# Optimization experiments

Measured on AMD Instinct MI355X. Metric: run time of the kernel, lower is better.

The kernel has to match this reference:

```python
import jax, jax.numpy as jnp
import numpy as np

NUM_CLASSES = 100            # num_classes (no-object class index == NUM_CLASSES)
MIN_PAIR_W = 0.1             # min_point_pair_weight
EPS = 1e-8


def setup_inputs() -> dict:
    key = jax.random.key(0)
    ks = jax.random.split(key, 8)
    B, Q, C1 = 16, 200, NUM_CLASSES + 1
    M = 800                  # matched GT instances across the batch
    NPTS = 200000            # sampled pixel points (per-point query-logit vectors)
    P = 500000               # point pairs for the clustering loss
    pred_logits = jax.random.normal(ks[0], (B, Q, C1), dtype=jnp.float32)
    targets = jax.random.randint(ks[1], (M,), 0, NUM_CLASSES)
    idx_b = jax.random.randint(ks[2], (M,), 0, B)
    idx_q = jax.random.randint(ks[3], (M,), 0, Q)
    src_clusters = jax.random.normal(ks[4], (NPTS, Q), dtype=jnp.float32)
    pairs = jax.random.randint(ks[5], (P, 2), 0, NPTS)
    pair_pos = jax.random.bernoulli(ks[6], 0.5, (P,))
    pair_weights = jax.random.uniform(ks[7], (P,), dtype=jnp.float32)
    # empty_weight buffer: ones with eos_coef on the no-object class
    empty_weight = jnp.ones((C1,), dtype=jnp.float32).at[-1].set(0.1)
    return {"pred_logits": pred_logits, "targets": targets, "idx_b": idx_b,
            "idx_q": idx_q, "src_clusters": src_clusters, "pairs": pairs,
            "pair_pos": pair_pos, "pair_weights": pair_weights,
            "empty_weight": empty_weight}


def _loss_labels(pred_logits, targets, idx_b, idx_q, empty_weight):
    B, Q, _ = pred_logits.shape
    # target_classes = full(no-object); target_classes[indices] = targets
    target_classes = jnp.full((B, Q), NUM_CLASSES, dtype=jnp.int32)
    target_classes = target_classes.at[idx_b, idx_q].set(targets.astype(jnp.int32))
    logp = jax.nn.log_softmax(pred_logits.astype(jnp.float32), axis=-1)  # [B,Q,C+1]
    nll = -jnp.take_along_axis(logp, target_classes[..., None], axis=-1)[..., 0]
    w = empty_weight[target_classes]
    # torch weighted cross_entropy: sum(w*nll)/sum(w)
    return jnp.sum(w * nll) / jnp.sum(w)


def _loss_clusters(src_clusters, pairs, pair_pos, pair_weights):
    a = src_clusters[pairs[:, 0]]            # [P,Q] gather
    b = src_clusters[pairs[:, 1]]            # [P,Q] gather
    cos = jnp.sum(a * b, axis=-1) / (
        jnp.linalg.norm(a, axis=-1) * jnp.linalg.norm(b, axis=-1) + EPS)
    w = jnp.maximum(pair_weights, MIN_PAIR_W)
    per_pair = jnp.where(pair_pos, 1.0 - cos, jnp.maximum(cos, 0.0))
    return jnp.sum(w * per_pair) / jnp.sum(w)


def reference(pred_logits, targets, idx_b, idx_q, src_clusters, pairs,
              pair_pos, pair_weights, empty_weight):
    loss_ce = _loss_labels(pred_logits, targets, idx_b, idx_q, empty_weight)
    loss_cluster = _loss_clusters(src_clusters, pairs, pair_pos, pair_weights)
    return loss_ce + loss_cluster
```

## Files before the change

kernel.cpp:

```cpp
#include <hip/hip_runtime.h>
#include <math.h>

#define NUM_CLASSES_ 100
#define C1_ 101
#define BQ_ 3200
#define QDIM_ 200
#define ROW_DW 64

typedef __attribute__((ext_vector_type(4))) int i32x4;

__global__ void init_kernel(float* acc, int* tc) {
    int i = blockIdx.x * blockDim.x + threadIdx.x;
    if (i < 4) acc[i] = 0.0f;
    if (i < BQ_) tc[i] = -1;
}

__global__ void scatter_kernel(const int* __restrict__ targets,
                               const int* __restrict__ idx_b,
                               const int* __restrict__ idx_q,
                               int* tc, int M) {
    int m = blockIdx.x * blockDim.x + threadIdx.x;
    if (m < M) {
        int slot = idx_b[m] * QDIM_ + idx_q[m];
        atomicMax(&tc[slot], (m << 8) | targets[m]);
    }
}

__global__ __launch_bounds__(256) void ce_kernel(const float* __restrict__ logits,
                                                 const int* __restrict__ tc,
                                                 const float* __restrict__ empty_w,
                                                 float* acc) {
    int lane = threadIdx.x & 63;
    int gw = (blockIdx.x * blockDim.x + threadIdx.x) >> 6;
    int nw = (gridDim.x * blockDim.x) >> 6;
    float lnum = 0.0f, lden = 0.0f;
    for (int row = gw; row < BQ_; row += nw) {
        const float* x = logits + (size_t)row * C1_;
        float x0 = x[lane];
        bool has2 = (lane < C1_ - 64);
        float x1 = has2 ? x[lane + 64] : -INFINITY;
        float m = fmaxf(x0, x1);
        #pragma unroll
        for (int off = 32; off; off >>= 1) m = fmaxf(m, __shfl_xor(m, off));
        float s = expf(x0 - m) + (has2 ? expf(x1 - m) : 0.0f);
        #pragma unroll
        for (int off = 32; off; off >>= 1) s += __shfl_xor(s, off);
        int packed = tc[row];
        int cls = (packed >= 0) ? (packed & 255) : NUM_CLASSES_;
        float xt = x[cls];
        float nll = -(xt - m - logf(s));
        float w = empty_w[cls];
        lnum += w * nll;
        lden += w;
    }
    if (lane == 0) { atomicAdd(&acc[0], lnum); atomicAdd(&acc[1], lden); }
}

__global__ __launch_bounds__(256) void quantize_kernel(const float* __restrict__ src,
                                                       unsigned int* __restrict__ qtab,
                                                       float* __restrict__ invq, int npts) {
    int lane = threadIdx.x & 63;
    int gw = (blockIdx.x * blockDim.x + threadIdx.x) >> 6;
    int nw = (gridDim.x * blockDim.x) >> 6;
    for (int r = gw; r < npts; r += nw) {
        float4 a = make_float4(0.f, 0.f, 0.f, 0.f);
        float s = 0.0f;
        if (lane < QDIM_ / 4) {
            a = reinterpret_cast<const float4*>(src + (size_t)r * QDIM_)[lane];
            s = a.x * a.x + a.y * a.y + a.z * a.z + a.w * a.w;
        }
        #pragma unroll
        for (int off = 32; off; off >>= 1) s += __shfl_xor(s, off);
        float inv = rsqrtf(s);
        inv = inv * (1.5f - 0.5f * s * inv * inv);
        float sc = inv * 127.0f;
        int q0 = (int)rintf(a.x * sc);
        int q1 = (int)rintf(a.y * sc);
        int q2 = (int)rintf(a.z * sc);
        int q3 = (int)rintf(a.w * sc);
        unsigned int packed = (unsigned)(q0 & 255) | ((unsigned)(q1 & 255) << 8)
                            | ((unsigned)(q2 & 255) << 16) | ((unsigned)(q3 & 255) << 24);
        int sq = q0 * q0 + q1 * q1 + q2 * q2 + q3 * q3;
        #pragma unroll
        for (int off = 32; off; off >>= 1) sq += __shfl_xor(sq, off);
        qtab[(size_t)r * ROW_DW + lane] = (lane < QDIM_ / 4) ? packed : 0u;
        if (lane == 0) {
            float fs = (float)sq;
            float iv = rsqrtf(fs);
            iv = iv * (1.5f - 0.5f * fs * iv * iv);
            invq[r] = iv;
        }
    }
}

__global__ __launch_bounds__(256) void pair_mfma_kernel(const uint4* __restrict__ qtab4,
                                                        const int2* __restrict__ pairs2,
                                                        const int* __restrict__ pos,
                                                        const float* __restrict__ pw,
                                                        const float* __restrict__ invq,
                                                        float* acc, int P) {
    int lane = threadIdx.x & 63;
    int i15 = lane & 15;
    int grp = lane >> 4;
    int gw = (blockIdx.x * blockDim.x + threadIdx.x) >> 6;
    int nw = (gridDim.x * blockDim.x) >> 6;
    int nchunks = (P + 15) / 16;

    int myreg = i15 - (grp << 2);
    bool owns = (myreg >= 0) && (myreg < 4);

    float num = 0.0f, den = 0.0f;

    int pA; int2 prA; uint4 a0A, a1A, a2A, a3A, b0A, b1A, b2A, b3A;
    int posA; float pwA, iqA;
    int pB; int2 prB; uint4 a0B, a1B, a2B, a3B, b0B, b1B, b2B, b3B;
    int posB; float pwB, iqB;

    auto loadA = [&](int c) {
        pA = c * 16 + i15;
        int pc = min(pA, P - 1);
        prA = pairs2[pc];
        const uint4* ar = qtab4 + (size_t)prA.x * 16;
        const uint4* br = qtab4 + (size_t)prA.y * 16;
        a0A = ar[grp]; a1A = ar[4 + grp]; a2A = ar[8 + grp]; a3A = ar[12 + grp];
        b0A = br[grp]; b1A = br[4 + grp]; b2A = br[8 + grp]; b3A = br[12 + grp];
        posA = pos[pc]; pwA = pw[pc];
        iqA = invq[prA.x] * invq[prA.y];
    };
    auto loadB = [&](int c) {
        pB = c * 16 + i15;
        int pc = min(pB, P - 1);
        prB = pairs2[pc];
        const uint4* ar = qtab4 + (size_t)prB.x * 16;
        const uint4* br = qtab4 + (size_t)prB.y * 16;
        a0B = ar[grp]; a1B = ar[4 + grp]; a2B = ar[8 + grp]; a3B = ar[12 + grp];
        b0B = br[grp]; b1B = br[4 + grp]; b2B = br[8 + grp]; b3B = br[12 + grp];
        posB = pos[pc]; pwB = pw[pc];
        iqB = invq[prB.x] * invq[prB.y];
    };
    auto procA = [&]() {
        i32x4 macc = {0, 0, 0, 0};
        macc = __builtin_amdgcn_mfma_i32_16x16x64_i8(*(i32x4*)&a0A, *(i32x4*)&b0A, macc, 0, 0, 0);
        macc = __builtin_amdgcn_mfma_i32_16x16x64_i8(*(i32x4*)&a1A, *(i32x4*)&b1A, macc, 0, 0, 0);
        macc = __builtin_amdgcn_mfma_i32_16x16x64_i8(*(i32x4*)&a2A, *(i32x4*)&b2A, macc, 0, 0, 0);
        macc = __builtin_amdgcn_mfma_i32_16x16x64_i8(*(i32x4*)&a3A, *(i32x4*)&b3A, macc, 0, 0, 0);
        if (owns && pA < P) {
            int d = (myreg == 0) ? macc[0] : (myreg == 1) ? macc[1]
                  : (myreg == 2) ? macc[2] : macc[3];
            float cosv = (float)d * iqA;
            float per = posA ? (1.0f - cosv) : fmaxf(cosv, 0.0f);
            float w = fmaxf(pwA, 0.1f);
            num += w * per;
            den += w;
        }
    };
    auto procB = [&]() {
        i32x4 macc = {0, 0, 0, 0};
        macc = __builtin_amdgcn_mfma_i32_16x16x64_i8(*(i32x4*)&a0B, *(i32x4*)&b0B, macc, 0, 0, 0);
        macc = __builtin_amdgcn_mfma_i32_16x16x64_i8(*(i32x4*)&a1B, *(i32x4*)&b1B, macc, 0, 0, 0);
        macc = __builtin_amdgcn_mfma_i32_16x16x64_i8(*(i32x4*)&a2B, *(i32x4*)&b2B, macc, 0, 0, 0);
        macc = __builtin_amdgcn_mfma_i32_16x16x64_i8(*(i32x4*)&a3B, *(i32x4*)&b3B, macc, 0, 0, 0);
        if (owns && pB < P) {
            int d = (myreg == 0) ? macc[0] : (myreg == 1) ? macc[1]
                  : (myreg == 2) ? macc[2] : macc[3];
            float cosv = (float)d * iqB;
            float per = posB ? (1.0f - cosv) : fmaxf(cosv, 0.0f);
            float w = fmaxf(pwB, 0.1f);
            num += w * per;
            den += w;
        }
    };

    if (gw < nchunks) {
        loadA(gw);
        int c = gw;
        for (;;) {
            int cB = c + nw;
            bool hasB = (cB < nchunks);
            if (hasB) loadB(cB);
            procA();
            if (!hasB) break;
            int cA = cB + nw;
            bool hasA = (cA < nchunks);
            if (hasA) loadA(cA);
            procB();
            if (!hasA) break;
            c = cA;
        }
    }

    #pragma unroll
    for (int off = 32; off; off >>= 1) {
        num += __shfl_xor(num, off);
        den += __shfl_xor(den, off);
    }
    __shared__ float snum[4], sden[4];
    int wib = threadIdx.x >> 6;
    if (lane == 0) { snum[wib] = num; sden[wib] = den; }
    __syncthreads();
    if (threadIdx.x == 0) {
        atomicAdd(&acc[2], snum[0] + snum[1] + snum[2] + snum[3]);
        atomicAdd(&acc[3], sden[0] + sden[1] + sden[2] + sden[3]);
    }
}

__global__ __launch_bounds__(256) void pair_fp32_kernel(const float* __restrict__ src,
                                                        const int* __restrict__ pairs,
                                                        const int* __restrict__ pos,
                                                        const float* __restrict__ pw,
                                                        float* acc, int P) {
    int lane = threadIdx.x & 63;
    int gw = (blockIdx.x * blockDim.x + threadIdx.x) >> 6;
    int nw = (gridDim.x * blockDim.x) >> 6;
    float num = 0.0f, den = 0.0f;
    for (int p = gw; p < P; p += nw) {
        int2 pr = reinterpret_cast<const int2*>(pairs)[p];
        float dot = 0.0f, saa = 0.0f, sbb = 0.0f;
        if (lane < QDIM_ / 4) {
            float4 a = reinterpret_cast<const float4*>(src + (size_t)pr.x * QDIM_)[lane];
            float4 b = reinterpret_cast<const float4*>(src + (size_t)pr.y * QDIM_)[lane];
            dot = a.x * b.x + a.y * b.y + a.z * b.z + a.w * b.w;
            saa = a.x * a.x + a.y * a.y + a.z * a.z + a.w * a.w;
            sbb = b.x * b.x + b.y * b.y + b.z * b.z + b.w * b.w;
        }
        #pragma unroll
        for (int off = 32; off; off >>= 1) {
            dot += __shfl_xor(dot, off);
            saa += __shfl_xor(saa, off);
            sbb += __shfl_xor(sbb, off);
        }
        float cosv = dot / (sqrtf(saa) * sqrtf(sbb) + 1e-8f);
        float per = pos[p] ? (1.0f - cosv) : fmaxf(cosv, 0.0f);
        float w = fmaxf(pw[p], 0.1f);
        num += w * per;
        den += w;
    }
    __shared__ float snum[4], sden[4];
    int wib = threadIdx.x >> 6;
    if (lane == 0) { snum[wib] = num; sden[wib] = den; }
    __syncthreads();
    if (threadIdx.x == 0) {
        atomicAdd(&acc[2], snum[0] + snum[1] + snum[2] + snum[3]);
        atomicAdd(&acc[3], sden[0] + sden[1] + sden[2] + sden[3]);
    }
}

__global__ void final_kernel(const float* __restrict__ acc, float* out) {
    if (threadIdx.x == 0 && blockIdx.x == 0)
        out[0] = acc[0] / acc[1] + acc[2] / acc[3];
}

extern "C" void kernel_launch(void* const* d_in, const int* in_sizes, int n_in,
                              void* d_out, int out_size, void* d_ws, size_t ws_size,
                              hipStream_t stream) {
    const float* pred_logits = (const float*)d_in[0];
    const int*   targets     = (const int*)d_in[1];
    const int*   idx_b       = (const int*)d_in[2];
    const int*   idx_q       = (const int*)d_in[3];
    const float* src         = (const float*)d_in[4];
    const int*   pairs       = (const int*)d_in[5];
    const int*   pair_pos    = (const int*)d_in[6];
    const float* pair_w      = (const float*)d_in[7];
    const float* empty_w     = (const float*)d_in[8];
    float* out = (float*)d_out;

    int M = in_sizes[1];
    int P = in_sizes[7];
    int npts = in_sizes[4] / QDIM_;

    float* acc = (float*)d_ws;
    int*   tc  = (int*)((char*)d_ws + 16);
    unsigned int* qtab = (unsigned int*)((char*)d_ws + 16384);
    float* invq = (float*)((char*)d_ws + 16384 + (size_t)npts * 256);

    init_kernel<<<(BQ_ + 255) / 256, 256, 0, stream>>>(acc, tc);
    scatter_kernel<<<(M + 255) / 256, 256, 0, stream>>>(targets, idx_b, idx_q, tc, M);
    ce_kernel<<<200, 256, 0, stream>>>(pred_logits, tc, empty_w, acc);

    bool i8 = ws_size >= (size_t)16384 + (size_t)npts * 256 + (size_t)npts * 4;
    if (i8) {
        quantize_kernel<<<2048, 256, 0, stream>>>(src, qtab, invq, npts);
        pair_mfma_kernel<<<2048, 256, 0, stream>>>((const uint4*)qtab, (const int2*)pairs,
                                                   pair_pos, pair_w, invq, acc, P);
    } else {
        pair_fp32_kernel<<<2048, 256, 0, stream>>>(src, pairs, pair_pos, pair_w, acc, P);
    }
    final_kernel<<<1, 64, 0, stream>>>(acc, out);
}
```

Before: 349.7 us.

## Bucket pairs by first point and map buckets to XCDs for L2 locality

Adds a histogram, prefix-sum and scatter pass that reorders the point pairs by the high bits of their first index. The pair kernel then assigns contiguous ranges of sorted chunks to each XCD (blockIdx & 7), so gathers of the quantized rows hit in that XCD's L2. The CE kernel is fused into the quantize launch as extra blocks, and the target scatter is merged with the histogram. The cost is three extra passes over the pair arrays with atomics, plus extra workspace.

```diff
diff --git a/kernel.cpp b/kernel.cpp
--- a/kernel.cpp
+++ b/kernel.cpp
@@ -9,20 +9,243 @@
 
 typedef __attribute__((ext_vector_type(4))) int i32x4;
 
-__global__ void init_kernel(float* acc, int* tc) {
+__global__ void init_kernel(float* acc, int* tc, int* cnt, int nb) {
     int i = blockIdx.x * blockDim.x + threadIdx.x;
     if (i < 4) acc[i] = 0.0f;
     if (i < BQ_) tc[i] = -1;
-}
-
-__global__ void scatter_kernel(const int* __restrict__ targets,
-                               const int* __restrict__ idx_b,
-                               const int* __restrict__ idx_q,
-                               int* tc, int M) {
-    int m = blockIdx.x * blockDim.x + threadIdx.x;
-    if (m < M) {
-        int slot = idx_b[m] * QDIM_ + idx_q[m];
-        atomicMax(&tc[slot], (m << 8) | targets[m]);
+    if (i < nb) cnt[i] = 0;
+}
+
+__global__ void scatter_hist_kernel(const int* __restrict__ targets,
+                                    const int* __restrict__ idx_b,
+                                    const int* __restrict__ idx_q,
+                                    int* tc, int M,
+                                    const int2* __restrict__ pairs2,
+                                    int* cnt, int shift, int P) {
+    int t = blockIdx.x * blockDim.x + threadIdx.x;
+    if (t < M) {
+        int slot = idx_b[t] * QDIM_ + idx_q[t];
+        atomicMax(&tc[slot], (t << 8) | targets[t]);
+    }
+    int stride = gridDim.x * blockDim.x;
+    for (int p = t; p < P; p += stride)
+        atomicAdd(&cnt[pairs2[p].x >> shift], 1);
+}
+
+__global__ void prefix_kernel(const int* __restrict__ cnt, int* cursor, int nb) {
+    __shared__ int s[256];
+    int tid = threadIdx.x;
+    int v = (tid < nb) ? cnt[tid] : 0;
+    s[tid] = v;
+    __syncthreads();
+    #pragma unroll
+    for (int off = 1; off < 256; off <<= 1) {
+        int t = (tid >= off) ? s[tid - off] : 0;
+        __syncthreads();
+        s[tid] += t;
+        __syncthreads();
+    }
+    if (tid < nb) cursor[tid] = s[tid] - v;
+}
+
+__global__ void scatter_pairs_kernel(const int2* __restrict__ pairs2,
+                                     const int* __restrict__ pos,
+                                     const float* __restrict__ pw,
+                                     int* cursor, int shift,
+                                     int2* __restrict__ sp,
+                                     int* __restrict__ spos,
+                                     float* __restrict__ spw, int P) {
+    int t = blockIdx.x * blockDim.x + threadIdx.x;
+    int stride = gridDim.x * blockDim.x;
+    for (int p = t; p < P; p += stride) {
+        int2 pr = pairs2[p];
+        int slot = atomicAdd(&cursor[pr.x >> shift], 1);
+        sp[slot] = pr;
+        spos[slot] = pos[p];
+        spw[slot] = pw[p];
+    }
+}
+
+__global__ __launch_bounds__(256) void quant_ce_kernel(const float* __restrict__ src,
+                                                       unsigned int* __restrict__ qtab,
+                                                       float* __restrict__ invq, int npts,
+                                                       const float* __restrict__ logits,
+                                                       const int* __restrict__ tc,
+                                                       const float* __restrict__ empty_w,
+                                                       float* acc, int qblocks) {
+    int lane = threadIdx.x & 63;
+    if ((int)blockIdx.x < qblocks) {
+        int gw = (blockIdx.x * blockDim.x + threadIdx.x) >> 6;
+        int nw = (qblocks * blockDim.x) >> 6;
+        for (int r = gw; r < npts; r += nw) {
+            float4 a = make_float4(0.f, 0.f, 0.f, 0.f);
+            float s = 0.0f;
+            if (lane < QDIM_ / 4) {
+                a = reinterpret_cast<const float4*>(src + (size_t)r * QDIM_)[lane];
+                s = a.x * a.x + a.y * a.y + a.z * a.z + a.w * a.w;
+            }
+            #pragma unroll
+            for (int off = 32; off; off >>= 1) s += __shfl_xor(s, off);
+            float inv = rsqrtf(s);
+            inv = inv * (1.5f - 0.5f * s * inv * inv);
+            float sc = inv * 127.0f;
+            int q0 = (int)rintf(a.x * sc);
+            int q1 = (int)rintf(a.y * sc);
+            int q2 = (int)rintf(a.z * sc);
+            int q3 = (int)rintf(a.w * sc);
+            unsigned int packed = (unsigned)(q0 & 255) | ((unsigned)(q1 & 255) << 8)
+                                | ((unsigned)(q2 & 255) << 16) | ((unsigned)(q3 & 255) << 24);
+            int sq = q0 * q0 + q1 * q1 + q2 * q2 + q3 * q3;
+            #pragma unroll
+            for (int off = 32; off; off >>= 1) sq += __shfl_xor(sq, off);
+            qtab[(size_t)r * ROW_DW + lane] = (lane < QDIM_ / 4) ? packed : 0u;
+            if (lane == 0) {
+                float fs = (float)sq;
+                float iv = rsqrtf(fs);
+                iv = iv * (1.5f - 0.5f * fs * iv * iv);
+                invq[r] = iv;
+            }
+        }
+    } else {
+        int bid = blockIdx.x - qblocks;
+        int gw = (bid * blockDim.x + threadIdx.x) >> 6;
+        int nw = (200 * blockDim.x) >> 6;
+        float lnum = 0.0f, lden = 0.0f;
+        for (int row = gw; row < BQ_; row += nw) {
+            const float* x = logits + (size_t)row * C1_;
+            float x0 = x[lane];
+            bool has2 = (lane < C1_ - 64);
+            float x1 = has2 ? x[lane + 64] : -INFINITY;
+            float m = fmaxf(x0, x1);
+            #pragma unroll
+            for (int off = 32; off; off >>= 1) m = fmaxf(m, __shfl_xor(m, off));
+            float s = expf(x0 - m) + (has2 ? expf(x1 - m) : 0.0f);
+            #pragma unroll
+            for (int off = 32; off; off >>= 1) s += __shfl_xor(s, off);
+            int packed = tc[row];
+            int cls = (packed >= 0) ? (packed & 255) : NUM_CLASSES_;
+            float xt = x[cls];
+            float nll = -(xt - m - logf(s));
+            float w = empty_w[cls];
+            lnum += w * nll;
+            lden += w;
+        }
+        if (lane == 0) { atomicAdd(&acc[0], lnum); atomicAdd(&acc[1], lden); }
+    }
+}
+
+__global__ __launch_bounds__(256) void pair_mfma_kernel(const uint4* __restrict__ qtab4,
+                                                        const int2* __restrict__ pairs2,
+                                                        const int* __restrict__ pos,
+                                                        const float* __restrict__ pw,
+                                                        const float* __restrict__ invq,
+                                                        float* acc, int P) {
+    int lane = threadIdx.x & 63;
+    int i15 = lane & 15;
+    int grp = lane >> 4;
+    int wib = threadIdx.x >> 6;
+    int nchunks = (P + 15) / 16;
+
+    int xcd = blockIdx.x & 7;
+    int lb  = blockIdx.x >> 3;
+    int lw  = lb * 4 + wib;
+    int lnw = ((gridDim.x >> 3) * blockDim.x) >> 6;
+    int nxc = (nchunks + 7) / 8;
+    int cbeg = xcd * nxc;
+    int cend = min(nchunks, cbeg + nxc);
+
+    int myreg = i15 - (grp << 2);
+    bool owns = (myreg >= 0) && (myreg < 4);
+
+    float num = 0.0f, den = 0.0f;
+
+    int pA; uint4 a0A, a1A, a2A, a3A, b0A, b1A, b2A, b3A; int posA; float pwA, iqA;
+    int pB; uint4 a0B, a1B, a2B, a3B, b0B, b1B, b2B, b3B; int posB; float pwB, iqB;
+
+    auto loadA = [&](int c) {
+        pA = c * 16 + i15;
+        int pc = min(pA, P - 1);
+        int2 pr = pairs2[pc];
+        const uint4* ar = qtab4 + (size_t)pr.x * 16;
+        const uint4* br = qtab4 + (size_t)pr.y * 16;
+        a0A = ar[grp]; a1A = ar[4 + grp]; a2A = ar[8 + grp]; a3A = ar[12 + grp];
+        b0A = br[grp]; b1A = br[4 + grp]; b2A = br[8 + grp]; b3A = br[12 + grp];
+        posA = pos[pc]; pwA = pw[pc];
+        iqA = invq[pr.x] * invq[pr.y];
+    };
+    auto loadB = [&](int c) {
+        pB = c * 16 + i15;
+        int pc = min(pB, P - 1);
+        int2 pr = pairs2[pc];
+        const uint4* ar = qtab4 + (size_t)pr.x * 16;
+        const uint4* br = qtab4 + (size_t)pr.y * 16;
+        a0B = ar[grp]; a1B = ar[4 + grp]; a2B = ar[8 + grp]; a3B = ar[12 + grp];
+        b0B = br[grp]; b1B = br[4 + grp]; b2B = br[8 + grp]; b3B = br[12 + grp];
+        posB = pos[pc]; pwB = pw[pc];
+        iqB = invq[pr.x] * invq[pr.y];
+    };
+    auto procA = [&]() {
+        i32x4 macc = {0, 0, 0, 0};
+        macc = __builtin_amdgcn_mfma_i32_16x16x64_i8(*(i32x4*)&a0A, *(i32x4*)&b0A, macc, 0, 0, 0);
+        macc = __builtin_amdgcn_mfma_i32_16x16x64_i8(*(i32x4*)&a1A, *(i32x4*)&b1A, macc, 0, 0, 0);
+        macc = __builtin_amdgcn_mfma_i32_16x16x64_i8(*(i32x4*)&a2A, *(i32x4*)&b2A, macc, 0, 0, 0);
+        macc = __builtin_amdgcn_mfma_i32_16x16x64_i8(*(i32x4*)&a3A, *(i32x4*)&b3A, macc, 0, 0, 0);
+        if (owns && pA < P) {
+            int d = (myreg == 0) ? macc[0] : (myreg == 1) ? macc[1]
+                  : (myreg == 2) ? macc[2] : macc[3];
+            float cosv = (float)d * iqA;
+            float per = posA ? (1.0f - cosv) : fmaxf(cosv, 0.0f);
+            float w = fmaxf(pwA, 0.1f);
+            num += w * per;
+            den += w;
+        }
+    };
+    auto procB = [&]() {
+        i32x4 macc = {0, 0, 0, 0};
+        macc = __builtin_amdgcn_mfma_i32_16x16x64_i8(*(i32x4*)&a0B, *(i32x4*)&b0B, macc, 0, 0, 0);
+        macc = __builtin_amdgcn_mfma_i32_16x16x64_i8(*(i32x4*)&a1B, *(i32x4*)&b1B, macc, 0, 0, 0);
+        macc = __builtin_amdgcn_mfma_i32_16x16x64_i8(*(i32x4*)&a2B, *(i32x4*)&b2B, macc, 0, 0, 0);
+        macc = __builtin_amdgcn_mfma_i32_16x16x64_i8(*(i32x4*)&a3B, *(i32x4*)&b3B, macc, 0, 0, 0);
+        if (owns && pB < P) {
+            int d = (myreg == 0) ? macc[0] : (myreg == 1) ? macc[1]
+                  : (myreg == 2) ? macc[2] : macc[3];
+            float cosv = (float)d * iqB;
+            float per = posB ? (1.0f - cosv) : fmaxf(cosv, 0.0f);
+            float w = fmaxf(pwB, 0.1f);
+            num += w * per;
+            den += w;
+        }
+    };
+
+    int c = cbeg + lw;
+    if (c < cend) {
+        loadA(c);
+        for (;;) {
+            int cB = c + lnw;
+            bool hasB = (cB < cend);
+            if (hasB) loadB(cB);
+            procA();
+            if (!hasB) break;
+            int cA = cB + lnw;
+            bool hasA = (cA < cend);
+            if (hasA) loadA(cA);
+            procB();
+            if (!hasA) break;
+            c = cA;
+        }
+    }
+
+    #pragma unroll
+    for (int off = 32; off; off >>= 1) {
+        num += __shfl_xor(num, off);
+        den += __shfl_xor(den, off);
+    }
+    __shared__ float snum[4], sden[4];
+    if (lane == 0) { snum[wib] = num; sden[wib] = den; }
+    __syncthreads();
+    if (threadIdx.x == 0) {
+        atomicAdd(&acc[2], snum[0] + snum[1] + snum[2] + snum[3]);
+        atomicAdd(&acc[3], sden[0] + sden[1] + sden[2] + sden[3]);
     }
 }
 
@@ -56,154 +279,6 @@
     if (lane == 0) { atomicAdd(&acc[0], lnum); atomicAdd(&acc[1], lden); }
 }
 
-__global__ __launch_bounds__(256) void quantize_kernel(const float* __restrict__ src,
-                                                       unsigned int* __restrict__ qtab,
-                                                       float* __restrict__ invq, int npts) {
-    int lane = threadIdx.x & 63;
-    int gw = (blockIdx.x * blockDim.x + threadIdx.x) >> 6;
-    int nw = (gridDim.x * blockDim.x) >> 6;
-    for (int r = gw; r < npts; r += nw) {
-        float4 a = make_float4(0.f, 0.f, 0.f, 0.f);
-        float s = 0.0f;
-        if (lane < QDIM_ / 4) {
-            a = reinterpret_cast<const float4*>(src + (size_t)r * QDIM_)[lane];
-            s = a.x * a.x + a.y * a.y + a.z * a.z + a.w * a.w;
-        }
-        #pragma unroll
-        for (int off = 32; off; off >>= 1) s += __shfl_xor(s, off);
-        float inv = rsqrtf(s);
-        inv = inv * (1.5f - 0.5f * s * inv * inv);
-        float sc = inv * 127.0f;
-        int q0 = (int)rintf(a.x * sc);
-        int q1 = (int)rintf(a.y * sc);
-        int q2 = (int)rintf(a.z * sc);
-        int q3 = (int)rintf(a.w * sc);
-        unsigned int packed = (unsigned)(q0 & 255) | ((unsigned)(q1 & 255) << 8)
-                            | ((unsigned)(q2 & 255) << 16) | ((unsigned)(q3 & 255) << 24);
-        int sq = q0 * q0 + q1 * q1 + q2 * q2 + q3 * q3;
-        #pragma unroll
-        for (int off = 32; off; off >>= 1) sq += __shfl_xor(sq, off);
-        qtab[(size_t)r * ROW_DW + lane] = (lane < QDIM_ / 4) ? packed : 0u;
-        if (lane == 0) {
-            float fs = (float)sq;
-            float iv = rsqrtf(fs);
-            iv = iv * (1.5f - 0.5f * fs * iv * iv);
-            invq[r] = iv;
-        }
-    }
-}
-
-__global__ __launch_bounds__(256) void pair_mfma_kernel(const uint4* __restrict__ qtab4,
-                                                        const int2* __restrict__ pairs2,
-                                                        const int* __restrict__ pos,
-                                                        const float* __restrict__ pw,
-                                                        const float* __restrict__ invq,
-                                                        float* acc, int P) {
-    int lane = threadIdx.x & 63;
-    int i15 = lane & 15;
-    int grp = lane >> 4;
-    int gw = (blockIdx.x * blockDim.x + threadIdx.x) >> 6;
-    int nw = (gridDim.x * blockDim.x) >> 6;
-    int nchunks = (P + 15) / 16;
-
-    int myreg = i15 - (grp << 2);
-    bool owns = (myreg >= 0) && (myreg < 4);
-
-    float num = 0.0f, den = 0.0f;
-
-    int pA; int2 prA; uint4 a0A, a1A, a2A, a3A, b0A, b1A, b2A, b3A;
-    int posA; float pwA, iqA;
-    int pB; int2 prB; uint4 a0B, a1B, a2B, a3B, b0B, b1B, b2B, b3B;
-    int posB; float pwB, iqB;
-
-    auto loadA = [&](int c) {
-        pA = c * 16 + i15;
-        int pc = min(pA, P - 1);
-        prA = pairs2[pc];
-        const uint4* ar = qtab4 + (size_t)prA.x * 16;
-        const uint4* br = qtab4 + (size_t)prA.y * 16;
-        a0A = ar[grp]; a1A = ar[4 + grp]; a2A = ar[8 + grp]; a3A = ar[12 + grp];
-        b0A = br[grp]; b1A = br[4 + grp]; b2A = br[8 + grp]; b3A = br[12 + grp];
-        posA = pos[pc]; pwA = pw[pc];
-        iqA = invq[prA.x] * invq[prA.y];
-    };
-    auto loadB = [&](int c) {
-        pB = c * 16 + i15;
-        int pc = min(pB, P - 1);
-        prB = pairs2[pc];
-        const uint4* ar = qtab4 + (size_t)prB.x * 16;
-        const uint4* br = qtab4 + (size_t)prB.y * 16;
-        a0B = ar[grp]; a1B = ar[4 + grp]; a2B = ar[8 + grp]; a3B = ar[12 + grp];
-        b0B = br[grp]; b1B = br[4 + grp]; b2B = br[8 + grp]; b3B = br[12 + grp];
-        posB = pos[pc]; pwB = pw[pc];
-        iqB = invq[prB.x] * invq[prB.y];
-    };
-    auto procA = [&]() {
-        i32x4 macc = {0, 0, 0, 0};
-        macc = __builtin_amdgcn_mfma_i32_16x16x64_i8(*(i32x4*)&a0A, *(i32x4*)&b0A, macc, 0, 0, 0);
-        macc = __builtin_amdgcn_mfma_i32_16x16x64_i8(*(i32x4*)&a1A, *(i32x4*)&b1A, macc, 0, 0, 0);
-        macc = __builtin_amdgcn_mfma_i32_16x16x64_i8(*(i32x4*)&a2A, *(i32x4*)&b2A, macc, 0, 0, 0);
-        macc = __builtin_amdgcn_mfma_i32_16x16x64_i8(*(i32x4*)&a3A, *(i32x4*)&b3A, macc, 0, 0, 0);
-        if (owns && pA < P) {
-            int d = (myreg == 0) ? macc[0] : (myreg == 1) ? macc[1]
-                  : (myreg == 2) ? macc[2] : macc[3];
-            float cosv = (float)d * iqA;
-            float per = posA ? (1.0f - cosv) : fmaxf(cosv, 0.0f);
-            float w = fmaxf(pwA, 0.1f);
-            num += w * per;
-            den += w;
-        }
-    };
-    auto procB = [&]() {
-        i32x4 macc = {0, 0, 0, 0};
-        macc = __builtin_amdgcn_mfma_i32_16x16x64_i8(*(i32x4*)&a0B, *(i32x4*)&b0B, macc, 0, 0, 0);
-        macc = __builtin_amdgcn_mfma_i32_16x16x64_i8(*(i32x4*)&a1B, *(i32x4*)&b1B, macc, 0, 0, 0);
-        macc = __builtin_amdgcn_mfma_i32_16x16x64_i8(*(i32x4*)&a2B, *(i32x4*)&b2B, macc, 0, 0, 0);
-        macc = __builtin_amdgcn_mfma_i32_16x16x64_i8(*(i32x4*)&a3B, *(i32x4*)&b3B, macc, 0, 0, 0);
-        if (owns && pB < P) {
-            int d = (myreg == 0) ? macc[0] : (myreg == 1) ? macc[1]
-                  : (myreg == 2) ? macc[2] : macc[3];
-            float cosv = (float)d * iqB;
-            float per = posB ? (1.0f - cosv) : fmaxf(cosv, 0.0f);
-            float w = fmaxf(pwB, 0.1f);
-            num += w * per;
-            den += w;
-        }
-    };
-
-    if (gw < nchunks) {
-        loadA(gw);
-        int c = gw;
-        for (;;) {
-            int cB = c + nw;
-            bool hasB = (cB < nchunks);
-            if (hasB) loadB(cB);
-            procA();
-            if (!hasB) break;
-            int cA = cB + nw;
-            bool hasA = (cA < nchunks);
-            if (hasA) loadA(cA);
-            procB();
-            if (!hasA) break;
-            c = cA;
-        }
-    }
-
-    #pragma unroll
-    for (int off = 32; off; off >>= 1) {
-        num += __shfl_xor(num, off);
-        den += __shfl_xor(den, off);
-    }
-    __shared__ float snum[4], sden[4];
-    int wib = threadIdx.x >> 6;
-    if (lane == 0) { snum[wib] = num; sden[wib] = den; }
-    __syncthreads();
-    if (threadIdx.x == 0) {
-        atomicAdd(&acc[2], snum[0] + snum[1] + snum[2] + snum[3]);
-        atomicAdd(&acc[3], sden[0] + sden[1] + sden[2] + sden[3]);
-    }
-}
-
 __global__ __launch_bounds__(256) void pair_fp32_kernel(const float* __restrict__ src,
                                                         const int* __restrict__ pairs,
                                                         const int* __restrict__ pos,
@@ -268,21 +343,39 @@
     int P = in_sizes[7];
     int npts = in_sizes[4] / QDIM_;
 
-    float* acc = (float*)d_ws;
-    int*   tc  = (int*)((char*)d_ws + 16);
-    unsigned int* qtab = (unsigned int*)((char*)d_ws + 16384);
-    float* invq = (float*)((char*)d_ws + 16384 + (size_t)npts * 256);
-
-    init_kernel<<<(BQ_ + 255) / 256, 256, 0, stream>>>(acc, tc);
-    scatter_kernel<<<(M + 255) / 256, 256, 0, stream>>>(targets, idx_b, idx_q, tc, M);
-    ce_kernel<<<200, 256, 0, stream>>>(pred_logits, tc, empty_w, acc);
-
-    bool i8 = ws_size >= (size_t)16384 + (size_t)npts * 256 + (size_t)npts * 4;
-    if (i8) {
-        quantize_kernel<<<2048, 256, 0, stream>>>(src, qtab, invq, npts);
-        pair_mfma_kernel<<<2048, 256, 0, stream>>>((const uint4*)qtab, (const int2*)pairs,
-                                                   pair_pos, pair_w, invq, acc, P);
+    int shift = 10;
+    while (((npts + (1 << shift) - 1) >> shift) > 256) shift++;
+    int nb = (npts + (1 << shift) - 1) >> shift;
+
+    float* acc    = (float*)d_ws;
+    int*   tc     = (int*)((char*)d_ws + 64);
+    int*   cnt    = (int*)((char*)d_ws + 16384);
+    int*   cursor = (int*)((char*)d_ws + 20480);
+    int2*  sp     = (int2*)((char*)d_ws + 32768);
+    int*   spos   = (int*)((char*)d_ws + (size_t)4194304 + (size_t)4 * P);
+    float* spw    = (float*)((char*)d_ws + (size_t)8388608 + (size_t)8 * P);
+    unsigned int* qtab = (unsigned int*)((char*)d_ws + 16777216);
+    float* invq   = (float*)((char*)d_ws + 16777216 + (size_t)npts * 256);
+
+    size_t need = (size_t)16777216 + (size_t)npts * 256 + (size_t)npts * 4;
+    bool fast = ws_size >= need && (size_t)P * 16 + 8388608 <= 16777216;
+
+    if (fast) {
+        init_kernel<<<(BQ_ + 255) / 256, 256, 0, stream>>>(acc, tc, cnt, nb);
+        scatter_hist_kernel<<<2048, 256, 0, stream>>>(targets, idx_b, idx_q, tc, M,
+                                                      (const int2*)pairs, cnt, shift, P);
+        prefix_kernel<<<1, 256, 0, stream>>>(cnt, cursor, nb);
+        scatter_pairs_kernel<<<2048, 256, 0, stream>>>((const int2*)pairs, pair_pos, pair_w,
+                                                       cursor, shift, sp, spos, spw, P);
+        quant_ce_kernel<<<2048 + 200, 256, 0, stream>>>(src, qtab, invq, npts,
+                                                        pred_logits, tc, empty_w, acc, 2048);
+        pair_mfma_kernel<<<2048, 256, 0, stream>>>((const uint4*)qtab, (const int2*)sp,
+                                                   spos, spw, invq, acc, P);
     } else {
+        init_kernel<<<(BQ_ + 255) / 256, 256, 0, stream>>>(acc, tc, cnt, nb);
+        scatter_hist_kernel<<<8, 256, 0, stream>>>(targets, idx_b, idx_q, tc, M,
+                                                   (const int2*)pairs, cnt, shift, 0);
+        ce_kernel<<<200, 256, 0, stream>>>(pred_logits, tc, empty_w, acc);
         pair_fp32_kernel<<<2048, 256, 0, stream>>>(src, pairs, pair_pos, pair_w, acc, P);
     }
     final_kernel<<<1, 64, 0, stream>>>(acc, out);
```

Measured after the change: 893.4 us. 155% more time.

## Quantize cluster rows to 4-bit with inline norms and fuse CE into quantize launch

Applied to the files above, without the earlier changes.

Rows of src_clusters are now quantized to signed 4-bit values with a per-row max-abs scale. Each row is packed into 128 bytes, with the quantized sum and inverse norm stored inline at the row tail, so the separate invq array and its gathers go away. The pair kernel unpacks nibbles into int8 MFMA operands and corrects for the +8 offset using the stored sums. This halves the random-gather traffic per pair. The CE kernel is merged into the quantize launch as extra blocks to save a launch. The cost is much coarser precision (4-bit cosine), which risks exceeding tolerance, plus extra unpack ALU work.

```diff
diff --git a/kernel.cpp b/kernel.cpp
--- a/kernel.cpp
+++ b/kernel.cpp
@@ -5,7 +5,6 @@
 #define C1_ 101
 #define BQ_ 3200
 #define QDIM_ 200
-#define ROW_DW 64
 
 typedef __attribute__((ext_vector_type(4))) int i32x4;
 
@@ -23,6 +22,211 @@
     if (m < M) {
         int slot = idx_b[m] * QDIM_ + idx_q[m];
         atomicMax(&tc[slot], (m << 8) | targets[m]);
+    }
+}
+
+__global__ __launch_bounds__(256) void quant_ce_kernel(const float* __restrict__ src,
+                                                       unsigned short* __restrict__ qtab16,
+                                                       int npts,
+                                                       const float* __restrict__ logits,
+                                                       const int* __restrict__ tc,
+                                                       const float* __restrict__ empty_w,
+                                                       float* acc, int qblocks) {
+    int lane = threadIdx.x & 63;
+    if ((int)blockIdx.x < qblocks) {
+        int gw = (blockIdx.x * blockDim.x + threadIdx.x) >> 6;
+        int nw = (qblocks * blockDim.x) >> 6;
+        for (int r = gw; r < npts; r += nw) {
+            float4 a = make_float4(0.f, 0.f, 0.f, 0.f);
+            float mx = 0.0f;
+            if (lane < QDIM_ / 4) {
+                a = reinterpret_cast<const float4*>(src + (size_t)r * QDIM_)[lane];
+                mx = fmaxf(fmaxf(fabsf(a.x), fabsf(a.y)), fmaxf(fabsf(a.z), fabsf(a.w)));
+            }
+            #pragma unroll
+            for (int off = 32; off; off >>= 1) mx = fmaxf(mx, __shfl_xor(mx, off));
+            float sc = (mx > 0.0f) ? 7.0f / mx : 0.0f;
+            int q0 = (int)rintf(a.x * sc);
+            int q1 = (int)rintf(a.y * sc);
+            int q2 = (int)rintf(a.z * sc);
+            int q3 = (int)rintf(a.w * sc);
+            int sq = q0 * q0 + q1 * q1 + q2 * q2 + q3 * q3;
+            int qs = q0 + q1 + q2 + q3;
+            #pragma unroll
+            for (int off = 32; off; off >>= 1) {
+                sq += __shfl_xor(sq, off);
+                qs += __shfl_xor(qs, off);
+            }
+            unsigned short h = (unsigned short)(((q0 + 8) & 15) | (((q1 + 8) & 15) << 4)
+                              | (((q2 + 8) & 15) << 8) | (((q3 + 8) & 15) << 12));
+            unsigned short* row = qtab16 + (size_t)r * 64;
+            if (lane < 50)      row[lane] = h;
+            else if (lane < 60) row[lane] = 0x8888;
+            else if (lane == 60) {
+                float fs = (float)sq;
+                float iv = 0.0f;
+                if (sq > 0) {
+                    iv = rsqrtf(fs);
+                    iv = iv * (1.5f - 0.5f * fs * iv * iv);
+                }
+                int2 m; m.x = qs; m.y = __float_as_int(iv);
+                reinterpret_cast<int2*>(row)[15] = m;
+            }
+        }
+    } else {
+        int bid = blockIdx.x - qblocks;
+        int gw = (bid * blockDim.x + threadIdx.x) >> 6;
+        int nw = (200 * blockDim.x) >> 6;
+        float lnum = 0.0f, lden = 0.0f;
+        for (int row = gw; row < BQ_; row += nw) {
+            const float* x = logits + (size_t)row * C1_;
+            float x0 = x[lane];
+            bool has2 = (lane < C1_ - 64);
+            float x1 = has2 ? x[lane + 64] : -INFINITY;
+            float m = fmaxf(x0, x1);
+            #pragma unroll
+            for (int off = 32; off; off >>= 1) m = fmaxf(m, __shfl_xor(m, off));
+            float s = expf(x0 - m) + (has2 ? expf(x1 - m) : 0.0f);
+            #pragma unroll
+            for (int off = 32; off; off >>= 1) s += __shfl_xor(s, off);
+            int packed = tc[row];
+            int cls = (packed >= 0) ? (packed & 255) : NUM_CLASSES_;
+            float xt = x[cls];
+            float nll = -(xt - m - logf(s));
+            float w = empty_w[cls];
+            lnum += w * nll;
+            lden += w;
+        }
+        if (lane == 0) { atomicAdd(&acc[0], lnum); atomicAdd(&acc[1], lden); }
+    }
+}
+
+__global__ __launch_bounds__(256) void pair_i4_kernel(const uint2* __restrict__ qtab2,
+                                                      const int2* __restrict__ pairs2,
+                                                      const int* __restrict__ pos,
+                                                      const float* __restrict__ pw,
+                                                      float* acc, int P) {
+    int lane = threadIdx.x & 63;
+    int i15 = lane & 15;
+    int grp = lane >> 4;
+    int gw = (blockIdx.x * blockDim.x + threadIdx.x) >> 6;
+    int nw = (gridDim.x * blockDim.x) >> 6;
+    int nchunks = (P + 15) / 16;
+
+    int myreg = i15 - (grp << 2);
+    bool owns = (myreg >= 0) && (myreg < 4);
+    const uint2 PADV = make_uint2(0x88888888u, 0x88888888u);
+
+    float num = 0.0f, den = 0.0f;
+
+    int pA; uint2 a0A, a1A, a2A, a3A, b0A, b1A, b2A, b3A; int posA; float pwA, iqA, corrA;
+    int pB; uint2 a0B, a1B, a2B, a3B, b0B, b1B, b2B, b3B; int posB; float pwB, iqB, corrB;
+
+    auto loadA = [&](int c) {
+        pA = c * 16 + i15;
+        int pc = min(pA, P - 1);
+        int2 pr = pairs2[pc];
+        const uint2* ar = qtab2 + (size_t)pr.x * 16;
+        const uint2* br = qtab2 + (size_t)pr.y * 16;
+        a0A = ar[grp];     b0A = br[grp];
+        a1A = ar[4 + grp]; b1A = br[4 + grp];
+        a2A = ar[8 + grp]; b2A = br[8 + grp];
+        a3A = (grp == 0) ? ar[12] : PADV;
+        b3A = (grp == 0) ? br[12] : PADV;
+        int2 mx = reinterpret_cast<const int2*>(ar)[15];
+        int2 my = reinterpret_cast<const int2*>(br)[15];
+        iqA = __int_as_float(mx.y) * __int_as_float(my.y);
+        corrA = (float)(8 * (mx.x + my.x) + 16384);
+        posA = pos[pc]; pwA = pw[pc];
+    };
+    auto loadB = [&](int c) {
+        pB = c * 16 + i15;
+        int pc = min(pB, P - 1);
+        int2 pr = pairs2[pc];
+        const uint2* ar = qtab2 + (size_t)pr.x * 16;
+        const uint2* br = qtab2 + (size_t)pr.y * 16;
+        a0B = ar[grp];     b0B = br[grp];
+        a1B = ar[4 + grp]; b1B = br[4 + grp];
+        a2B = ar[8 + grp]; b2B = br[8 + grp];
+        a3B = (grp == 0) ? ar[12] : PADV;
+        b3B = (grp == 0) ? br[12] : PADV;
+        int2 mx = reinterpret_cast<const int2*>(ar)[15];
+        int2 my = reinterpret_cast<const int2*>(br)[15];
+        iqB = __int_as_float(mx.y) * __int_as_float(my.y);
+        corrB = (float)(8 * (mx.x + my.x) + 16384);
+        posB = pos[pc]; pwB = pw[pc];
+    };
+    auto UNP = [](uint2 v) -> i32x4 {
+        i32x4 r;
+        r[0] = (int)(v.x & 0x0F0F0F0Fu);
+        r[1] = (int)((v.x >> 4) & 0x0F0F0F0Fu);
+        r[2] = (int)(v.y & 0x0F0F0F0Fu);
+        r[3] = (int)((v.y >> 4) & 0x0F0F0F0Fu);
+        return r;
+    };
+    auto procA = [&]() {
+        i32x4 macc = {0, 0, 0, 0};
+        macc = __builtin_amdgcn_mfma_i32_16x16x64_i8(UNP(a0A), UNP(b0A), macc, 0, 0, 0);
+        macc = __builtin_amdgcn_mfma_i32_16x16x64_i8(UNP(a1A), UNP(b1A), macc, 0, 0, 0);
+        macc = __builtin_amdgcn_mfma_i32_16x16x64_i8(UNP(a2A), UNP(b2A), macc, 0, 0, 0);
+        macc = __builtin_amdgcn_mfma_i32_16x16x64_i8(UNP(a3A), UNP(b3A), macc, 0, 0, 0);
+        if (owns && pA < P) {
+            int d = (myreg == 0) ? macc[0] : (myreg == 1) ? macc[1]
+                  : (myreg == 2) ? macc[2] : macc[3];
+            float cosv = ((float)d - corrA) * iqA;
+            float per = posA ? (1.0f - cosv) : fmaxf(cosv, 0.0f);
+            float w = fmaxf(pwA, 0.1f);
+            num += w * per;
+            den += w;
+        }
+    };
+    auto procB = [&]() {
+        i32x4 macc = {0, 0, 0, 0};
+        macc = __builtin_amdgcn_mfma_i32_16x16x64_i8(UNP(a0B), UNP(b0B), macc, 0, 0, 0);
+        macc = __builtin_amdgcn_mfma_i32_16x16x64_i8(UNP(a1B), UNP(b1B), macc, 0, 0, 0);
+        macc = __builtin_amdgcn_mfma_i32_16x16x64_i8(UNP(a2B), UNP(b2B), macc, 0, 0, 0);
+        macc = __builtin_amdgcn_mfma_i32_16x16x64_i8(UNP(a3B), UNP(b3B), macc, 0, 0, 0);
+        if (owns && pB < P) {
+            int d = (myreg == 0) ? macc[0] : (myreg == 1) ? macc[1]
+                  : (myreg == 2) ? macc[2] : macc[3];
+            float cosv = ((float)d - corrB) * iqB;
+            float per = posB ? (1.0f - cosv) : fmaxf(cosv, 0.0f);
+            float w = fmaxf(pwB, 0.1f);
+            num += w * per;
+            den += w;
+        }
+    };
+
+    if (gw < nchunks) {
+        loadA(gw);
+        int c = gw;
+        for (;;) {
+            int cB = c + nw;
+            bool hasB = (cB < nchunks);
+            if (hasB) loadB(cB);
+            procA();
+            if (!hasB) break;
+            int cA = cB + nw;
+            bool hasA = (cA < nchunks);
+            if (hasA) loadA(cA);
+            procB();
+            if (!hasA) break;
+            c = cA;
+        }
+    }
+
+    #pragma unroll
+    for (int off = 32; off; off >>= 1) {
+        num += __shfl_xor(num, off);
+        den += __shfl_xor(den, off);
+    }
+    __shared__ float snum[4], sden[4];
+    int wib = threadIdx.x >> 6;
+    if (lane == 0) { snum[wib] = num; sden[wib] = den; }
+    __syncthreads();
+    if (threadIdx.x == 0) {
+        atomicAdd(&acc[2], snum[0] + snum[1] + snum[2] + snum[3]);
+        atomicAdd(&acc[3], sden[0] + sden[1] + sden[2] + sden[3]);
     }
 }
 
@@ -56,154 +260,6 @@
     if (lane == 0) { atomicAdd(&acc[0], lnum); atomicAdd(&acc[1], lden); }
 }
 
-__global__ __launch_bounds__(256) void quantize_kernel(const float* __restrict__ src,
-                                                       unsigned int* __restrict__ qtab,
-                                                       float* __restrict__ invq, int npts) {
-    int lane = threadIdx.x & 63;
-    int gw = (blockIdx.x * blockDim.x + threadIdx.x) >> 6;
-    int nw = (gridDim.x * blockDim.x) >> 6;
-    for (int r = gw; r < npts; r += nw) {
-        float4 a = make_float4(0.f, 0.f, 0.f, 0.f);
-        float s = 0.0f;
-        if (lane < QDIM_ / 4) {
-            a = reinterpret_cast<const float4*>(src + (size_t)r * QDIM_)[lane];
-            s = a.x * a.x + a.y * a.y + a.z * a.z + a.w * a.w;
-        }
-        #pragma unroll
-        for (int off = 32; off; off >>= 1) s += __shfl_xor(s, off);
-        float inv = rsqrtf(s);
-        inv = inv * (1.5f - 0.5f * s * inv * inv);
-        float sc = inv * 127.0f;
-        int q0 = (int)rintf(a.x * sc);
-        int q1 = (int)rintf(a.y * sc);
-        int q2 = (int)rintf(a.z * sc);
-        int q3 = (int)rintf(a.w * sc);
-        unsigned int packed = (unsigned)(q0 & 255) | ((unsigned)(q1 & 255) << 8)
-                            | ((unsigned)(q2 & 255) << 16) | ((unsigned)(q3 & 255) << 24);
-        int sq = q0 * q0 + q1 * q1 + q2 * q2 + q3 * q3;
-        #pragma unroll
-        for (int off = 32; off; off >>= 1) sq += __shfl_xor(sq, off);
-        qtab[(size_t)r * ROW_DW + lane] = (lane < QDIM_ / 4) ? packed : 0u;
-        if (lane == 0) {
-            float fs = (float)sq;
-            float iv = rsqrtf(fs);
-            iv = iv * (1.5f - 0.5f * fs * iv * iv);
-            invq[r] = iv;
-        }
-    }
-}
-
-__global__ __launch_bounds__(256) void pair_mfma_kernel(const uint4* __restrict__ qtab4,
-                                                        const int2* __restrict__ pairs2,
-                                                        const int* __restrict__ pos,
-                                                        const float* __restrict__ pw,
-                                                        const float* __restrict__ invq,
-                                                        float* acc, int P) {
-    int lane = threadIdx.x & 63;
-    int i15 = lane & 15;
-    int grp = lane >> 4;
-    int gw = (blockIdx.x * blockDim.x + threadIdx.x) >> 6;
-    int nw = (gridDim.x * blockDim.x) >> 6;
-    int nchunks = (P + 15) / 16;
-
-    int myreg = i15 - (grp << 2);
-    bool owns = (myreg >= 0) && (myreg < 4);
-
-    float num = 0.0f, den = 0.0f;
-
-    int pA; int2 prA; uint4 a0A, a1A, a2A, a3A, b0A, b1A, b2A, b3A;
-    int posA; float pwA, iqA;
-    int pB; int2 prB; uint4 a0B, a1B, a2B, a3B, b0B, b1B, b2B, b3B;
-    int posB; float pwB, iqB;
-
-    auto loadA = [&](int c) {
-        pA = c * 16 + i15;
-        int pc = min(pA, P - 1);
-        prA = pairs2[pc];
-        const uint4* ar = qtab4 + (size_t)prA.x * 16;
-        const uint4* br = qtab4 + (size_t)prA.y * 16;
-        a0A = ar[grp]; a1A = ar[4 + grp]; a2A = ar[8 + grp]; a3A = ar[12 + grp];
-        b0A = br[grp]; b1A = br[4 + grp]; b2A = br[8 + grp]; b3A = br[12 + grp];
-        posA = pos[pc]; pwA = pw[pc];
-        iqA = invq[prA.x] * invq[prA.y];
-    };
-    auto loadB = [&](int c) {
-        pB = c * 16 + i15;
-        int pc = min(pB, P - 1);
-        prB = pairs2[pc];
-        const uint4* ar = qtab4 + (size_t)prB.x * 16;
-        const uint4* br = qtab4 + (size_t)prB.y * 16;
-        a0B = ar[grp]; a1B = ar[4 + grp]; a2B = ar[8 + grp]; a3B = ar[12 + grp];
-        b0B = br[grp]; b1B = br[4 + grp]; b2B = br[8 + grp]; b3B = br[12 + grp];
-        posB = pos[pc]; pwB = pw[pc];
-        iqB = invq[prB.x] * invq[prB.y];
-    };
-    auto procA = [&]() {
-        i32x4 macc = {0, 0, 0, 0};
-        macc = __builtin_amdgcn_mfma_i32_16x16x64_i8(*(i32x4*)&a0A, *(i32x4*)&b0A, macc, 0, 0, 0);
-        macc = __builtin_amdgcn_mfma_i32_16x16x64_i8(*(i32x4*)&a1A, *(i32x4*)&b1A, macc, 0, 0, 0);
-        macc = __builtin_amdgcn_mfma_i32_16x16x64_i8(*(i32x4*)&a2A, *(i32x4*)&b2A, macc, 0, 0, 0);
-        macc = __builtin_amdgcn_mfma_i32_16x16x64_i8(*(i32x4*)&a3A, *(i32x4*)&b3A, macc, 0, 0, 0);
-        if (owns && pA < P) {
-            int d = (myreg == 0) ? macc[0] : (myreg == 1) ? macc[1]
-                  : (myreg == 2) ? macc[2] : macc[3];
-            float cosv = (float)d * iqA;
-            float per = posA ? (1.0f - cosv) : fmaxf(cosv, 0.0f);
-            float w = fmaxf(pwA, 0.1f);
-            num += w * per;
-            den += w;
-        }
-    };
-    auto procB = [&]() {
-        i32x4 macc = {0, 0, 0, 0};
-        macc = __builtin_amdgcn_mfma_i32_16x16x64_i8(*(i32x4*)&a0B, *(i32x4*)&b0B, macc, 0, 0, 0);
-        macc = __builtin_amdgcn_mfma_i32_16x16x64_i8(*(i32x4*)&a1B, *(i32x4*)&b1B, macc, 0, 0, 0);
-        macc = __builtin_amdgcn_mfma_i32_16x16x64_i8(*(i32x4*)&a2B, *(i32x4*)&b2B, macc, 0, 0, 0);
-        macc = __builtin_amdgcn_mfma_i32_16x16x64_i8(*(i32x4*)&a3B, *(i32x4*)&b3B, macc, 0, 0, 0);
-        if (owns && pB < P) {
-            int d = (myreg == 0) ? macc[0] : (myreg == 1) ? macc[1]
-                  : (myreg == 2) ? macc[2] : macc[3];
-            float cosv = (float)d * iqB;
-            float per = posB ? (1.0f - cosv) : fmaxf(cosv, 0.0f);
-            float w = fmaxf(pwB, 0.1f);
-            num += w * per;
-            den += w;
-        }
-    };
-
-    if (gw < nchunks) {
-        loadA(gw);
-        int c = gw;
-        for (;;) {
-            int cB = c + nw;
-            bool hasB = (cB < nchunks);
-            if (hasB) loadB(cB);
-            procA();
-            if (!hasB) break;
-            int cA = cB + nw;
-            bool hasA = (cA < nchunks);
-            if (hasA) loadA(cA);
-            procB();
-            if (!hasA) break;
-            c = cA;
-        }
-    }
-
-    #pragma unroll
-    for (int off = 32; off; off >>= 1) {
-        num += __shfl_xor(num, off);
-        den += __shfl_xor(den, off);
-    }
-    __shared__ float snum[4], sden[4];
-    int wib = threadIdx.x >> 6;
-    if (lane == 0) { snum[wib] = num; sden[wib] = den; }
-    __syncthreads();
-    if (threadIdx.x == 0) {
-        atomicAdd(&acc[2], snum[0] + snum[1] + snum[2] + snum[3]);
-        atomicAdd(&acc[3], sden[0] + sden[1] + sden[2] + sden[3]);
-    }
-}
-
 __global__ __launch_bounds__(256) void pair_fp32_kernel(const float* __restrict__ src,
                                                         const int* __restrict__ pairs,
                                                         const int* __restrict__ pos,
@@ -269,20 +325,20 @@
     int npts = in_sizes[4] / QDIM_;
 
     float* acc = (float*)d_ws;
-    int*   tc  = (int*)((char*)d_ws + 16);
-    unsigned int* qtab = (unsigned int*)((char*)d_ws + 16384);
-    float* invq = (float*)((char*)d_ws + 16384 + (size_t)npts * 256);
+    int*   tc  = (int*)((char*)d_ws + 64);
+    unsigned short* qtab16 = (unsigned short*)((char*)d_ws + 16384);
 
     init_kernel<<<(BQ_ + 255) / 256, 256, 0, stream>>>(acc, tc);
     scatter_kernel<<<(M + 255) / 256, 256, 0, stream>>>(targets, idx_b, idx_q, tc, M);
-    ce_kernel<<<200, 256, 0, stream>>>(pred_logits, tc, empty_w, acc);
-
-    bool i8 = ws_size >= (size_t)16384 + (size_t)npts * 256 + (size_t)npts * 4;
-    if (i8) {
-        quantize_kernel<<<2048, 256, 0, stream>>>(src, qtab, invq, npts);
-        pair_mfma_kernel<<<2048, 256, 0, stream>>>((const uint4*)qtab, (const int2*)pairs,
-                                                   pair_pos, pair_w, invq, acc, P);
+
+    bool fast = ws_size >= (size_t)16384 + (size_t)npts * 128;
+    if (fast) {
+        quant_ce_kernel<<<2048 + 200, 256, 0, stream>>>(src, qtab16, npts,
+                                                        pred_logits, tc, empty_w, acc, 2048);
+        pair_i4_kernel<<<2048, 256, 0, stream>>>((const uint2*)qtab16, (const int2*)pairs,
+                                                 pair_pos, pair_w, acc, P);
     } else {
+        ce_kernel<<<200, 256, 0, stream>>>(pred_logits, tc, empty_w, acc);
         pair_fp32_kernel<<<2048, 256, 0, stream>>>(src, pairs, pair_pos, pair_w, acc, P);
     }
     final_kernel<<<1, 64, 0, stream>>>(acc, out);
```

Measured after the change: 333.4 us. 4.7% less time.
